# Optimization experiments

Measured on AMD Instinct MI355X. Metric: run time of the kernel, lower is better.

The kernel has to match this reference:

```python
import jax, jax.numpy as jnp
import numpy as np

N = 100000      # nodes
E = 3200000     # edges
G = 1024        # graphs in the batch
D_IN = 128      # input feature dim
H = 64          # hidden dim
BN_EPS = 1e-5


def _linear_init(key, fan_in, shape):
    bound = 1.0 / np.sqrt(fan_in)
    return jax.random.uniform(key, shape, jnp.float32, -bound, bound)


def setup_inputs() -> dict:
    key = jax.random.key(0)
    ks = jax.random.split(key, 16)
    x = jax.random.normal(ks[0], (N, D_IN), jnp.float32)
    edge_index = jax.random.randint(ks[1], (2, E), 0, N, dtype=jnp.int32)
    batch = jnp.sort(jax.random.randint(ks[2], (N,), 0, G, dtype=jnp.int32))
    inp = {"x": x, "edge_index": edge_index, "batch": batch}
    # layer 0 MLP: Linear(D_IN,H) -> ReLU -> BN(H) -> Linear(H,H) -> ReLU
    inp["W1_0"] = _linear_init(ks[3], D_IN, (D_IN, H))
    inp["b1_0"] = _linear_init(ks[4], D_IN, (H,))
    inp["g_0"] = jnp.ones((H,), jnp.float32)
    inp["be_0"] = jnp.zeros((H,), jnp.float32)
    inp["W2_0"] = _linear_init(ks[5], H, (H, H))
    inp["b2_0"] = _linear_init(ks[6], H, (H,))
    # layer 1 MLP: Linear(H,H) -> ReLU -> BN(H) -> Linear(H,H) -> ReLU
    inp["W1_1"] = _linear_init(ks[7], H, (H, H))
    inp["b1_1"] = _linear_init(ks[8], H, (H,))
    inp["g_1"] = jnp.ones((H,), jnp.float32)
    inp["be_1"] = jnp.zeros((H,), jnp.float32)
    inp["W2_1"] = _linear_init(ks[9], H, (H, H))
    inp["b2_1"] = _linear_init(ks[10], H, (H,))
    return inp


def _mlp(h, W1, b1, g, be, W2, b2):
    h = jnp.maximum(h @ W1 + b1, 0.0)
    mu = h.mean(axis=0)                      # BatchNorm1d (training: batch stats)
    var = h.var(axis=0)                      # biased variance, as torch normalizes
    h = g * (h - mu) * jax.lax.rsqrt(var + BN_EPS) + be
    return jnp.maximum(h @ W2 + b2, 0.0)


def _gin(h, src, dst, mlp_params):
    # GINConv, eps=0: out = mlp(x_i + sum_{j->i} x_j)
    agg = jax.ops.segment_sum(h[src], dst, num_segments=N)
    return _mlp(h + agg, *mlp_params)


def reference(x, edge_index, batch,
              W1_0, b1_0, g_0, be_0, W2_0, b2_0,
              W1_1, b1_1, g_1, be_1, W2_1, b2_1):
    src, dst = edge_index[0], edge_index[1]
    h = _gin(x, src, dst, (W1_0, b1_0, g_0, be_0, W2_0, b2_0))
    h = _gin(h, src, dst, (W1_1, b1_1, g_1, be_1, W2_1, b2_1))
    x_g = jax.ops.segment_sum(h, batch, num_segments=G)  # global add pooling
    return (x_g, h)
```

## Files before the change

### kernel.cpp

```cpp
#include <hip/hip_runtime.h>

static inline int cdiv_ll(long long a, long long b){ return (int)((a + b - 1) / b); }

#define EB_CHUNK 8192
#define NPB 256
#define MAXNB 512

__device__ __forceinline__ float bf2f(unsigned short h) {
  unsigned u = (unsigned)h << 16;
  return __uint_as_float(u);
}
__device__ __forceinline__ unsigned short f2bf(float f) {
  unsigned u = __float_as_uint(f);
  u += 0x7FFF + ((u >> 16) & 1);
  return (unsigned short)(u >> 16);
}

template<int K, bool IN_BF16, bool RELU_IN, bool RELU_OUT, bool BIAS, bool OUT_BF16>
__global__ __launch_bounds__(256) void gemm64x64(
    const void* __restrict__ Xv, const float* __restrict__ W,
    const float* __restrict__ bias, void* __restrict__ Yv, int M)
{
  __shared__ float Wl[K * 64];
  __shared__ float XT[64 * 68];
  const float* Xf = (const float*)Xv;
  const unsigned short* Xh = (const unsigned short*)Xv;

  for (int i = threadIdx.x; i < K * 16; i += 256)
    reinterpret_cast<float4*>(Wl)[i] = reinterpret_cast<const float4*>(W)[i];

  const int tr = threadIdx.x >> 4;
  const int tc = threadIdx.x & 15;
  const long long rb = (long long)blockIdx.x * 64;

  float acc[4][4] = {};

  for (int ch = 0; ch < K / 64; ++ch) {
    const int c0 = ch * 64;
    __syncthreads();
    for (int f = threadIdx.x; f < 1024; f += 256) {
      int r = f >> 4, k0 = (f & 15) * 4;
      float4 v = make_float4(0.f, 0.f, 0.f, 0.f);
      if (rb + r < M) {
        if (IN_BF16) {
          ushort4 h = *reinterpret_cast<const ushort4*>(Xh + (rb + r) * K + c0 + k0);
          v.x = bf2f(h.x); v.y = bf2f(h.y); v.z = bf2f(h.z); v.w = bf2f(h.w);
        } else {
          v = *reinterpret_cast<const float4*>(Xf + (rb + r) * K + c0 + k0);
        }
        if (RELU_IN) {
          v.x = fmaxf(v.x, 0.f); v.y = fmaxf(v.y, 0.f);
          v.z = fmaxf(v.z, 0.f); v.w = fmaxf(v.w, 0.f);
        }
      }
      XT[(k0 + 0) * 68 + r] = v.x;
      XT[(k0 + 1) * 68 + r] = v.y;
      XT[(k0 + 2) * 68 + r] = v.z;
      XT[(k0 + 3) * 68 + r] = v.w;
    }
    __syncthreads();
    #pragma unroll 8
    for (int k = 0; k < 64; ++k) {
      float4 xa = *reinterpret_cast<const float4*>(&XT[k * 68 + 4 * tr]);
      float4 wb = *reinterpret_cast<const float4*>(&Wl[(c0 + k) * 64 + 4 * tc]);
      acc[0][0] = fmaf(xa.x, wb.x, acc[0][0]); acc[0][1] = fmaf(xa.x, wb.y, acc[0][1]);
      acc[0][2] = fmaf(xa.x, wb.z, acc[0][2]); acc[0][3] = fmaf(xa.x, wb.w, acc[0][3]);
      acc[1][0] = fmaf(xa.y, wb.x, acc[1][0]); acc[1][1] = fmaf(xa.y, wb.y, acc[1][1]);
      acc[1][2] = fmaf(xa.y, wb.z, acc[1][2]); acc[1][3] = fmaf(xa.y, wb.w, acc[1][3]);
      acc[2][0] = fmaf(xa.z, wb.x, acc[2][0]); acc[2][1] = fmaf(xa.z, wb.y, acc[2][1]);
      acc[2][2] = fmaf(xa.z, wb.z, acc[2][2]); acc[2][3] = fmaf(xa.z, wb.w, acc[2][3]);
      acc[3][0] = fmaf(xa.w, wb.x, acc[3][0]); acc[3][1] = fmaf(xa.w, wb.y, acc[3][1]);
      acc[3][2] = fmaf(xa.w, wb.z, acc[3][2]); acc[3][3] = fmaf(xa.w, wb.w, acc[3][3]);
    }
  }

  float4 bb = make_float4(0.f, 0.f, 0.f, 0.f);
  if (BIAS) bb = *reinterpret_cast<const float4*>(bias + 4 * tc);
  #pragma unroll
  for (int rr = 0; rr < 4; ++rr) {
    long long row = rb + 4 * tr + rr;
    if (row < M) {
      float4 o = make_float4(acc[rr][0] + bb.x, acc[rr][1] + bb.y,
                             acc[rr][2] + bb.z, acc[rr][3] + bb.w);
      if (RELU_OUT) {
        o.x = fmaxf(o.x, 0.f); o.y = fmaxf(o.y, 0.f);
        o.z = fmaxf(o.z, 0.f); o.w = fmaxf(o.w, 0.f);
      }
      if (OUT_BF16) {
        ushort4 h; h.x = f2bf(o.x); h.y = f2bf(o.y); h.z = f2bf(o.z); h.w = f2bf(o.w);
        *reinterpret_cast<ushort4*>((unsigned short*)Yv + row * 64 + 4 * tc) = h;
      } else {
        *reinterpret_cast<float4*>((float*)Yv + row * 64 + 4 * tc) = o;
      }
    }
  }
}

__global__ __launch_bounds__(256) void gemm_dual(
    const float* __restrict__ A, const float* __restrict__ Wa64,
    const float* __restrict__ ba, const float* __restrict__ Wb64,
    unsigned short* __restrict__ P, int M)
{
  __shared__ float Wa[64 * 64];
  __shared__ float Wb[64 * 64];
  __shared__ float XT[64 * 68];
  for (int i = threadIdx.x; i < 1024; i += 256) {
    reinterpret_cast<float4*>(Wa)[i] = reinterpret_cast<const float4*>(Wa64)[i];
    reinterpret_cast<float4*>(Wb)[i] = reinterpret_cast<const float4*>(Wb64)[i];
  }
  const int tr = threadIdx.x >> 4;
  const int tc = threadIdx.x & 15;
  const long long rb = (long long)blockIdx.x * 64;

  for (int f = threadIdx.x; f < 1024; f += 256) {
    int r = f >> 4, k0 = (f & 15) * 4;
    float4 v = make_float4(0.f, 0.f, 0.f, 0.f);
    if (rb + r < M) {
      v = *reinterpret_cast<const float4*>(A + (rb + r) * 64 + k0);
      v.x = fmaxf(v.x, 0.f); v.y = fmaxf(v.y, 0.f);
      v.z = fmaxf(v.z, 0.f); v.w = fmaxf(v.w, 0.f);
    }
    XT[(k0 + 0) * 68 + r] = v.x;
    XT[(k0 + 1) * 68 + r] = v.y;
    XT[(k0 + 2) * 68 + r] = v.z;
    XT[(k0 + 3) * 68 + r] = v.w;
  }
  __syncthreads();

  float acc[4][4] = {};
  #pragma unroll 8
  for (int k = 0; k < 64; ++k) {
    float4 xa = *reinterpret_cast<const float4*>(&XT[k * 68 + 4 * tr]);
    float4 wb = *reinterpret_cast<const float4*>(&Wa[k * 64 + 4 * tc]);
    acc[0][0] = fmaf(xa.x, wb.x, acc[0][0]); acc[0][1] = fmaf(xa.x, wb.y, acc[0][1]);
    acc[0][2] = fmaf(xa.x, wb.z, acc[0][2]); acc[0][3] = fmaf(xa.x, wb.w, acc[0][3]);
    acc[1][0] = fmaf(xa.y, wb.x, acc[1][0]); acc[1][1] = fmaf(xa.y, wb.y, acc[1][1]);
    acc[1][2] = fmaf(xa.y, wb.z, acc[1][2]); acc[1][3] = fmaf(xa.y, wb.w, acc[1][3]);
    acc[2][0] = fmaf(xa.z, wb.x, acc[2][0]); acc[2][1] = fmaf(xa.z, wb.y, acc[2][1]);
    acc[2][2] = fmaf(xa.z, wb.z, acc[2][2]); acc[2][3] = fmaf(xa.z, wb.w, acc[2][3]);
    acc[3][0] = fmaf(xa.w, wb.x, acc[3][0]); acc[3][1] = fmaf(xa.w, wb.y, acc[3][1]);
    acc[3][2] = fmaf(xa.w, wb.z, acc[3][2]); acc[3][3] = fmaf(xa.w, wb.w, acc[3][3]);
  }
  float4 bb = *reinterpret_cast<const float4*>(ba + 4 * tc);
  float h[4][4];
  #pragma unroll
  for (int rr = 0; rr < 4; ++rr) {
    h[rr][0] = fmaxf(acc[rr][0] + bb.x, 0.f);
    h[rr][1] = fmaxf(acc[rr][1] + bb.y, 0.f);
    h[rr][2] = fmaxf(acc[rr][2] + bb.z, 0.f);
    h[rr][3] = fmaxf(acc[rr][3] + bb.w, 0.f);
  }
  __syncthreads();
  #pragma unroll
  for (int cc = 0; cc < 4; ++cc) {
    float4 v = make_float4(h[0][cc], h[1][cc], h[2][cc], h[3][cc]);
    *reinterpret_cast<float4*>(&XT[(4 * tc + cc) * 68 + 4 * tr]) = v;
  }
  __syncthreads();

  float ac2[4][4] = {};
  #pragma unroll 8
  for (int k = 0; k < 64; ++k) {
    float4 xa = *reinterpret_cast<const float4*>(&XT[k * 68 + 4 * tr]);
    float4 wb = *reinterpret_cast<const float4*>(&Wb[k * 64 + 4 * tc]);
    ac2[0][0] = fmaf(xa.x, wb.x, ac2[0][0]); ac2[0][1] = fmaf(xa.x, wb.y, ac2[0][1]);
    ac2[0][2] = fmaf(xa.x, wb.z, ac2[0][2]); ac2[0][3] = fmaf(xa.x, wb.w, ac2[0][3]);
    ac2[1][0] = fmaf(xa.y, wb.x, ac2[1][0]); ac2[1][1] = fmaf(xa.y, wb.y, ac2[1][1]);
    ac2[1][2] = fmaf(xa.y, wb.z, ac2[1][2]); ac2[1][3] = fmaf(xa.y, wb.w, ac2[1][3]);
    ac2[2][0] = fmaf(xa.z, wb.x, ac2[2][0]); ac2[2][1] = fmaf(xa.z, wb.y, ac2[2][1]);
    ac2[2][2] = fmaf(xa.z, wb.z, ac2[2][2]); ac2[2][3] = fmaf(xa.z, wb.w, ac2[2][3]);
    ac2[3][0] = fmaf(xa.w, wb.x, ac2[3][0]); ac2[3][1] = fmaf(xa.w, wb.y, ac2[3][1]);
    ac2[3][2] = fmaf(xa.w, wb.z, ac2[3][2]); ac2[3][3] = fmaf(xa.w, wb.w, ac2[3][3]);
  }
  #pragma unroll
  for (int rr = 0; rr < 4; ++rr) {
    long long row = rb + 4 * tr + rr;
    if (row < M) {
      ushort4 hh;
      hh.x = f2bf(ac2[rr][0]); hh.y = f2bf(ac2[rr][1]);
      hh.z = f2bf(ac2[rr][2]); hh.w = f2bf(ac2[rr][3]);
      *reinterpret_cast<ushort4*>(P + row * 64 + 4 * tc) = hh;
    }
  }
}

__global__ __launch_bounds__(256) void part_hist(
    const int* __restrict__ dst, int* __restrict__ blockHist,
    int E, int NB, int nblocksB)
{
  __shared__ int hist[MAXNB];
  for (int i = threadIdx.x; i < NB; i += 256) hist[i] = 0;
  __syncthreads();
  int base = blockIdx.x * EB_CHUNK;
  int end = min(base + EB_CHUNK, E);
  for (int e = base + threadIdx.x; e < end; e += 256)
    atomicAdd(&hist[dst[e] >> 8], 1);
  __syncthreads();
  for (int i = threadIdx.x; i < NB; i += 256)
    blockHist[(long long)i * nblocksB + blockIdx.x] = hist[i];
}

__global__ __launch_bounds__(256) void scan_bucket_blocks(
    int* __restrict__ blockHist, int* __restrict__ bucketTotal, int nblocksB)
{
  int* row = blockHist + (long long)blockIdx.x * nblocksB;
  __shared__ int tsum[256];
  int v[4]; int local = 0;
  int i0 = threadIdx.x * 4;
  #pragma unroll
  for (int k = 0; k < 4; ++k) { int g = i0 + k; v[k] = (g < nblocksB) ? row[g] : 0; local += v[k]; }
  tsum[threadIdx.x] = local;
  __syncthreads();
  for (int off = 1; off < 256; off <<= 1) {
    int y = (threadIdx.x >= off) ? tsum[threadIdx.x - off] : 0;
    __syncthreads();
    tsum[threadIdx.x] += y;
    __syncthreads();
  }
  int pref = tsum[threadIdx.x] - local;
  #pragma unroll
  for (int k = 0; k < 4; ++k) { int g = i0 + k; if (g < nblocksB) { row[g] = pref; pref += v[k]; } }
  if (threadIdx.x == 255) bucketTotal[blockIdx.x] = tsum[255];
}

__global__ __launch_bounds__(512) void scan_buckets(
    const int* __restrict__ bucketTotal, int* __restrict__ bucketBase, int NB)
{
  __shared__ int tsum[512];
  int t = threadIdx.x;
  int v = (t < NB) ? bucketTotal[t] : 0;
  tsum[t] = v;
  __syncthreads();
  for (int off = 1; off < 512; off <<= 1) {
    int y = (t >= off) ? tsum[t - off] : 0;
    __syncthreads();
    tsum[t] += y;
    __syncthreads();
  }
  if (t < NB) bucketBase[t] = tsum[t] - v;
  if (t == NB - 1) bucketBase[NB] = tsum[t];
}

__global__ __launch_bounds__(256) void part_scatter(
    const int* __restrict__ src, const int* __restrict__ dst,
    const int* __restrict__ blockHist, const int* __restrict__ bucketBase,
    unsigned* __restrict__ ebuf, int E, int NB, int nblocksB)
{
  __shared__ int cursor[MAXNB];
  for (int i = threadIdx.x; i < NB; i += 256)
    cursor[i] = bucketBase[i] + blockHist[(long long)i * nblocksB + blockIdx.x];
  __syncthreads();
  int base = blockIdx.x * EB_CHUNK;
  int end = min(base + EB_CHUNK, E);
  for (int e = base + threadIdx.x; e < end; e += 256) {
    int s = src[e], d = dst[e];
    int p = atomicAdd(&cursor[d >> 8], 1);
    ebuf[p] = (unsigned)s | ((unsigned)(d & (NPB - 1)) << 24);
  }
}

__global__ __launch_bounds__(256) void bucket_csr(
    const unsigned* __restrict__ ebuf, const int* __restrict__ bucketBase,
    int* __restrict__ rowptr, int* __restrict__ col, int N, int NB)
{
  int b = blockIdx.x;
  int eb = bucketBase[b], ee = bucketBase[b + 1];
  int nodeBase = b * NPB;
  __shared__ int hist[NPB];
  __shared__ int tsum[NPB];
  __shared__ int cur[NPB];
  hist[threadIdx.x] = 0;
  __syncthreads();
  for (int e = eb + threadIdx.x; e < ee; e += 256)
    atomicAdd(&hist[ebuf[e] >> 24], 1);
  __syncthreads();
  int local = hist[threadIdx.x];
  tsum[threadIdx.x] = local;
  __syncthreads();
  for (int off = 1; off < 256; off <<= 1) {
    int y = (threadIdx.x >= off) ? tsum[threadIdx.x - off] : 0;
    __syncthreads();
    tsum[threadIdx.x] += y;
    __syncthreads();
  }
  int pref = tsum[threadIdx.x] - local;
  int node = nodeBase + threadIdx.x;
  if (node < N) rowptr[node] = eb + pref;
  if (b == NB - 1 && threadIdx.x == 0) rowptr[N] = ee;
  cur[threadIdx.x] = pref;
  __syncthreads();
  for (int e = eb + threadIdx.x; e < ee; e += 256) {
    unsigned w = ebuf[e];
    int l = (int)(w >> 24);
    int p = eb + atomicAdd(&cur[l], 1);
    col[p] = (int)(w & 0xFFFFFFu);
  }
}

__global__ __launch_bounds__(256) void gin_gather_bf16(
    const int* __restrict__ rowptr, const int* __restrict__ col,
    const unsigned short* __restrict__ P, const float* __restrict__ b1,
    float* __restrict__ A, float* __restrict__ stats, int N, int nodeStride)
{
  const int lane = threadIdx.x & 63;
  const int wv = threadIdx.x >> 6;
  const int q = lane >> 4;
  const int cl = lane & 15;
  float s[4] = {0.f, 0.f, 0.f, 0.f};
  float sq[4] = {0.f, 0.f, 0.f, 0.f};
  const float4 bb = *reinterpret_cast<const float4*>(b1 + 4 * cl);

  for (int node = blockIdx.x * 4 + wv; node < N; node += nodeStride) {
    const int beg = rowptr[node], end = rowptr[node + 1];
    float a0 = 0.f, a1 = 0.f, a2 = 0.f, a3 = 0.f;
    if (q == 1) {
      ushort4 h = *reinterpret_cast<const ushort4*>(P + (long long)node * 64 + 4 * cl);
      a0 = bf2f(h.x); a1 = bf2f(h.y); a2 = bf2f(h.z); a3 = bf2f(h.w);
    } else if (q == 2) {
      a0 = bb.x; a1 = bb.y; a2 = bb.z; a3 = bb.w;
    }
    int j = beg + q;
    for (; j + 12 < end; j += 16) {
      int rA = col[j], rB = col[j + 4], rC = col[j + 8], rD = col[j + 12];
      ushort4 hA = *reinterpret_cast<const ushort4*>(P + (long long)rA * 64 + 4 * cl);
      ushort4 hB = *reinterpret_cast<const ushort4*>(P + (long long)rB * 64 + 4 * cl);
      ushort4 hC = *reinterpret_cast<const ushort4*>(P + (long long)rC * 64 + 4 * cl);
      ushort4 hD = *reinterpret_cast<const ushort4*>(P + (long long)rD * 64 + 4 * cl);
      a0 += bf2f(hA.x); a1 += bf2f(hA.y); a2 += bf2f(hA.z); a3 += bf2f(hA.w);
      a0 += bf2f(hB.x); a1 += bf2f(hB.y); a2 += bf2f(hB.z); a3 += bf2f(hB.w);
      a0 += bf2f(hC.x); a1 += bf2f(hC.y); a2 += bf2f(hC.z); a3 += bf2f(hC.w);
      a0 += bf2f(hD.x); a1 += bf2f(hD.y); a2 += bf2f(hD.z); a3 += bf2f(hD.w);
    }
    for (; j < end; j += 4) {
      int rA = col[j];
      ushort4 hA = *reinterpret_cast<const ushort4*>(P + (long long)rA * 64 + 4 * cl);
      a0 += bf2f(hA.x); a1 += bf2f(hA.y); a2 += bf2f(hA.z); a3 += bf2f(hA.w);
    }
    a0 += __shfl_xor(a0, 16); a0 += __shfl_xor(a0, 32);
    a1 += __shfl_xor(a1, 16); a1 += __shfl_xor(a1, 32);
    a2 += __shfl_xor(a2, 16); a2 += __shfl_xor(a2, 32);
    a3 += __shfl_xor(a3, 16); a3 += __shfl_xor(a3, 32);
    if (q == 0) {
      *reinterpret_cast<float4*>(A + (long long)node * 64 + 4 * cl) =
          make_float4(a0, a1, a2, a3);
    } else if (q == 1) {
      float r0 = fmaxf(a0, 0.f), r1 = fmaxf(a1, 0.f);
      float r2 = fmaxf(a2, 0.f), r3 = fmaxf(a3, 0.f);
      s[0] += r0; s[1] += r1; s[2] += r2; s[3] += r3;
      sq[0] += r0 * r0; sq[1] += r1 * r1; sq[2] += r2 * r2; sq[3] += r3 * r3;
    }
  }

  __shared__ float st[4][16][8];
  if (q == 1) {
    st[wv][cl][0] = s[0]; st[wv][cl][1] = s[1]; st[wv][cl][2] = s[2]; st[wv][cl][3] = s[3];
    st[wv][cl][4] = sq[0]; st[wv][cl][5] = sq[1]; st[wv][cl][6] = sq[2]; st[wv][cl][7] = sq[3];
  }
  __syncthreads();
  if (threadIdx.x < 128) {
    int c = threadIdx.x;
    int colid = c & 63, part = c >> 6;
    int idx = (part ? 4 : 0) + (colid & 3);
    float v = st[0][colid >> 2][idx] + st[1][colid >> 2][idx]
            + st[2][colid >> 2][idx] + st[3][colid >> 2][idx];
    atomicAdd(&stats[c], v);
  }
}

__global__ void bn_fold(
    const float* __restrict__ stats, const float* __restrict__ g, const float* __restrict__ be,
    const float* __restrict__ W2, const float* __restrict__ b2,
    float* __restrict__ W2f, float* __restrict__ b2f, float invN)
{
  int j = threadIdx.x;
  __shared__ float sc[64], sh[64];
  float mu = stats[j] * invN;
  float var = stats[64 + j] * invN - mu * mu;
  float s = g[j] * rsqrtf(var + 1e-5f);
  sc[j] = s;
  sh[j] = be[j] - mu * s;
  __syncthreads();
  float acc = b2[j];
  for (int k = 0; k < 64; ++k) {
    float w = W2[k * 64 + j];
    W2f[k * 64 + j] = sc[k] * w;
    acc += sh[k] * w;
  }
  b2f[j] = acc;
}

__global__ __launch_bounds__(256) void pool_sorted(
    const float* __restrict__ Hf, const int* __restrict__ batch,
    float* __restrict__ out, int N, int G)
{
  int g = blockIdx.x * 4 + (threadIdx.x >> 6);
  int c = threadIdx.x & 63;
  if (g >= G) return;
  int lo = 0, hi = N;
  while (lo < hi) { int mid = (lo + hi) >> 1; if (batch[mid] < g) lo = mid + 1; else hi = mid; }
  int beg = lo;
  hi = N;
  while (lo < hi) { int mid = (lo + hi) >> 1; if (batch[mid] < g + 1) lo = mid + 1; else hi = mid; }
  int end = lo;
  float acc = 0.f;
  for (int r = beg; r < end; ++r) acc += Hf[(long long)r * 64 + c];
  out[(long long)g * 64 + c] = acc;
}

extern "C" void kernel_launch(void* const* d_in, const int* in_sizes, int n_in,
                              void* d_out, int out_size, void* d_ws, size_t ws_size,
                              hipStream_t stream) {
  const float* x      = (const float*)d_in[0];
  const int*   ei     = (const int*)d_in[1];
  const int*   batch  = (const int*)d_in[2];
  const float* W1_0 = (const float*)d_in[3];
  const float* b1_0 = (const float*)d_in[4];
  const float* g_0  = (const float*)d_in[5];
  const float* be_0 = (const float*)d_in[6];
  const float* W2_0 = (const float*)d_in[7];
  const float* b2_0 = (const float*)d_in[8];
  const float* W1_1 = (const float*)d_in[9];
  const float* b1_1 = (const float*)d_in[10];
  const float* g_1  = (const float*)d_in[11];
  const float* be_1 = (const float*)d_in[12];
  const float* W2_1 = (const float*)d_in[13];
  const float* b2_1 = (const float*)d_in[14];

  const int N = in_sizes[0] / 128;
  const int E = in_sizes[1] / 2;
  const int G = (out_size - N * 64) / 64;
  const int* srcI = ei;
  const int* dstI = ei + E;

  float* outG = (float*)d_out;
  float* outH = (float*)d_out + (long long)G * 64;

  const int NB = cdiv_ll(N, NPB);
  const int nblocksB = cdiv_ll(E, EB_CHUNK);

  char* w = (char*)d_ws;
  size_t r2 = (size_t)E * 4;
  if ((size_t)N * 64 * 2 > r2) r2 = (size_t)N * 64 * 2;
  unsigned* ebuf        = (unsigned*)w;
  unsigned short* Pbuf  = (unsigned short*)w;
  w += r2;
  int* col       = (int*)w; w += (size_t)E * 4;
  int* rowptr    = (int*)w; w += (size_t)(N + 1) * 4;
  int* blockHist = (int*)w; w += (size_t)NB * nblocksB * 4;
  int* bucketTotal = (int*)w; w += (size_t)NB * 4;
  int* bucketBase  = (int*)w; w += (size_t)(NB + 1) * 4;
  float* stats0 = (float*)w; w += 128 * 4;
  float* stats1 = (float*)w; w += 128 * 4;
  float* W2f0   = (float*)w; w += 64 * 64 * 4;
  float* b2f0   = (float*)w; w += 64 * 4;
  float* W2f1   = (float*)w; w += 64 * 64 * 4;
  float* b2f1   = (float*)w; w += 64 * 4;

  const int gemmGrid = cdiv_ll(N, 64);
  const int gatherGrid = 2048;

  hipMemsetAsync(stats0, 0, 256 * sizeof(float), stream);

  part_hist<<<nblocksB, 256, 0, stream>>>(dstI, blockHist, E, NB, nblocksB);
  scan_bucket_blocks<<<NB, 256, 0, stream>>>(blockHist, bucketTotal, nblocksB);
  scan_buckets<<<1, 512, 0, stream>>>(bucketTotal, bucketBase, NB);
  part_scatter<<<nblocksB, 256, 0, stream>>>(srcI, dstI, blockHist, bucketBase, ebuf, E, NB, nblocksB);
  bucket_csr<<<NB, 256, 0, stream>>>(ebuf, bucketBase, rowptr, col, N, NB);

  gemm64x64<128, false, false, false, false, true><<<gemmGrid, 256, 0, stream>>>(x, W1_0, nullptr, Pbuf, N);
  gin_gather_bf16<<<gatherGrid, 256, 0, stream>>>(rowptr, col, Pbuf, b1_0, outH, stats0, N, gatherGrid * 4);
  bn_fold<<<1, 64, 0, stream>>>(stats0, g_0, be_0, W2_0, b2_0, W2f0, b2f0, 1.0f / N);
  gemm_dual<<<gemmGrid, 256, 0, stream>>>(outH, W2f0, b2f0, W1_1, Pbuf, N);

  gin_gather_bf16<<<gatherGrid, 256, 0, stream>>>(rowptr, col, Pbuf, b1_1, outH, stats1, N, gatherGrid * 4);
  bn_fold<<<1, 64, 0, stream>>>(stats1, g_1, be_1, W2_1, b2_1, W2f1, b2f1, 1.0f / N);
  gemm64x64<64, false, true, true, true, false><<<gemmGrid, 256, 0, stream>>>(outH, W2f1, b2f1, outH, N);

  pool_sorted<<<cdiv_ll(G, 4), 256, 0, stream>>>(outH, batch, outG, N, G);
}
```

Before: 440.0 us.

## Switch dense GEMMs to bf16 MFMA and cache CSR bucket edges in LDS

Replaces the scalar fp32 FMA GEMM kernels with bf16 MFMA 16x16x32 kernels. Inputs and weights are converted to bf16 in swizzled LDS tiles, so the GEMMs run on the matrix cores. Separately, bucket_csr stages each bucket's edges in LDS when they fit, which avoids reading ebuf from global memory twice. The cost is reduced precision: inputs and the intermediate hidden layer in the dual GEMM are rounded to bf16, where before they were fp32.

```diff
diff --git a/kernel.cpp b/kernel.cpp
--- a/kernel.cpp
+++ b/kernel.cpp
@@ -5,6 +5,10 @@
 #define EB_CHUNK 8192
 #define NPB 256
 #define MAXNB 512
+#define CSR_LDS 10240
+
+typedef short bf16x8 __attribute__((ext_vector_type(8)));
+typedef float f32x4 __attribute__((ext_vector_type(4)));
 
 __device__ __forceinline__ float bf2f(unsigned short h) {
   unsigned u = (unsigned)h << 16;
@@ -16,170 +20,134 @@
   return (unsigned short)(u >> 16);
 }
 
-template<int K, bool IN_BF16, bool RELU_IN, bool RELU_OUT, bool BIAS, bool OUT_BF16>
-__global__ __launch_bounds__(256) void gemm64x64(
-    const void* __restrict__ Xv, const float* __restrict__ W,
-    const float* __restrict__ bias, void* __restrict__ Yv, int M)
-{
-  __shared__ float Wl[K * 64];
-  __shared__ float XT[64 * 68];
-  const float* Xf = (const float*)Xv;
-  const unsigned short* Xh = (const unsigned short*)Xv;
-
-  for (int i = threadIdx.x; i < K * 16; i += 256)
-    reinterpret_cast<float4*>(Wl)[i] = reinterpret_cast<const float4*>(W)[i];
-
-  const int tr = threadIdx.x >> 4;
-  const int tc = threadIdx.x & 15;
-  const long long rb = (long long)blockIdx.x * 64;
-
-  float acc[4][4] = {};
-
-  for (int ch = 0; ch < K / 64; ++ch) {
-    const int c0 = ch * 64;
-    __syncthreads();
-    for (int f = threadIdx.x; f < 1024; f += 256) {
-      int r = f >> 4, k0 = (f & 15) * 4;
-      float4 v = make_float4(0.f, 0.f, 0.f, 0.f);
-      if (rb + r < M) {
-        if (IN_BF16) {
-          ushort4 h = *reinterpret_cast<const ushort4*>(Xh + (rb + r) * K + c0 + k0);
-          v.x = bf2f(h.x); v.y = bf2f(h.y); v.z = bf2f(h.z); v.w = bf2f(h.w);
-        } else {
-          v = *reinterpret_cast<const float4*>(Xf + (rb + r) * K + c0 + k0);
-        }
-        if (RELU_IN) {
-          v.x = fmaxf(v.x, 0.f); v.y = fmaxf(v.y, 0.f);
-          v.z = fmaxf(v.z, 0.f); v.w = fmaxf(v.w, 0.f);
-        }
-      }
-      XT[(k0 + 0) * 68 + r] = v.x;
-      XT[(k0 + 1) * 68 + r] = v.y;
-      XT[(k0 + 2) * 68 + r] = v.z;
-      XT[(k0 + 3) * 68 + r] = v.w;
-    }
-    __syncthreads();
-    #pragma unroll 8
-    for (int k = 0; k < 64; ++k) {
-      float4 xa = *reinterpret_cast<const float4*>(&XT[k * 68 + 4 * tr]);
-      float4 wb = *reinterpret_cast<const float4*>(&Wl[(c0 + k) * 64 + 4 * tc]);
-      acc[0][0] = fmaf(xa.x, wb.x, acc[0][0]); acc[0][1] = fmaf(xa.x, wb.y, acc[0][1]);
-      acc[0][2] = fmaf(xa.x, wb.z, acc[0][2]); acc[0][3] = fmaf(xa.x, wb.w, acc[0][3]);
-      acc[1][0] = fmaf(xa.y, wb.x, acc[1][0]); acc[1][1] = fmaf(xa.y, wb.y, acc[1][1]);
-      acc[1][2] = fmaf(xa.y, wb.z, acc[1][2]); acc[1][3] = fmaf(xa.y, wb.w, acc[1][3]);
-      acc[2][0] = fmaf(xa.z, wb.x, acc[2][0]); acc[2][1] = fmaf(xa.z, wb.y, acc[2][1]);
-      acc[2][2] = fmaf(xa.z, wb.z, acc[2][2]); acc[2][3] = fmaf(xa.z, wb.w, acc[2][3]);
-      acc[3][0] = fmaf(xa.w, wb.x, acc[3][0]); acc[3][1] = fmaf(xa.w, wb.y, acc[3][1]);
-      acc[3][2] = fmaf(xa.w, wb.z, acc[3][2]); acc[3][3] = fmaf(xa.w, wb.w, acc[3][3]);
-    }
-  }
-
-  float4 bb = make_float4(0.f, 0.f, 0.f, 0.f);
-  if (BIAS) bb = *reinterpret_cast<const float4*>(bias + 4 * tc);
-  #pragma unroll
-  for (int rr = 0; rr < 4; ++rr) {
-    long long row = rb + 4 * tr + rr;
-    if (row < M) {
-      float4 o = make_float4(acc[rr][0] + bb.x, acc[rr][1] + bb.y,
-                             acc[rr][2] + bb.z, acc[rr][3] + bb.w);
-      if (RELU_OUT) {
-        o.x = fmaxf(o.x, 0.f); o.y = fmaxf(o.y, 0.f);
-        o.z = fmaxf(o.z, 0.f); o.w = fmaxf(o.w, 0.f);
-      }
-      if (OUT_BF16) {
-        ushort4 h; h.x = f2bf(o.x); h.y = f2bf(o.y); h.z = f2bf(o.z); h.w = f2bf(o.w);
-        *reinterpret_cast<ushort4*>((unsigned short*)Yv + row * 64 + 4 * tc) = h;
-      } else {
-        *reinterpret_cast<float4*>((float*)Yv + row * 64 + 4 * tc) = o;
-      }
-    }
-  }
-}
-
-__global__ __launch_bounds__(256) void gemm_dual(
-    const float* __restrict__ A, const float* __restrict__ Wa64,
-    const float* __restrict__ ba, const float* __restrict__ Wb64,
-    unsigned short* __restrict__ P, int M)
-{
-  __shared__ float Wa[64 * 64];
-  __shared__ float Wb[64 * 64];
-  __shared__ float XT[64 * 68];
-  for (int i = threadIdx.x; i < 1024; i += 256) {
-    reinterpret_cast<float4*>(Wa)[i] = reinterpret_cast<const float4*>(Wa64)[i];
-    reinterpret_cast<float4*>(Wb)[i] = reinterpret_cast<const float4*>(Wb64)[i];
-  }
-  const int tr = threadIdx.x >> 4;
-  const int tc = threadIdx.x & 15;
-  const long long rb = (long long)blockIdx.x * 64;
-
-  for (int f = threadIdx.x; f < 1024; f += 256) {
-    int r = f >> 4, k0 = (f & 15) * 4;
+#define SWZ(row, byteoff) ((byteoff) ^ (((row) & 7) << 4))
+
+template<int K, bool RELU>
+__device__ __forceinline__ void stage_x_bf16(
+    char* XlB, const float* __restrict__ X, long long rb, int M)
+{
+  for (int f = threadIdx.x; f < 16 * K; f += 256) {
+    int r = f / (K / 4), c4 = (f % (K / 4)) * 4;
     float4 v = make_float4(0.f, 0.f, 0.f, 0.f);
     if (rb + r < M) {
-      v = *reinterpret_cast<const float4*>(A + (rb + r) * 64 + k0);
-      v.x = fmaxf(v.x, 0.f); v.y = fmaxf(v.y, 0.f);
-      v.z = fmaxf(v.z, 0.f); v.w = fmaxf(v.w, 0.f);
-    }
-    XT[(k0 + 0) * 68 + r] = v.x;
-    XT[(k0 + 1) * 68 + r] = v.y;
-    XT[(k0 + 2) * 68 + r] = v.z;
-    XT[(k0 + 3) * 68 + r] = v.w;
-  }
-  __syncthreads();
-
-  float acc[4][4] = {};
-  #pragma unroll 8
-  for (int k = 0; k < 64; ++k) {
-    float4 xa = *reinterpret_cast<const float4*>(&XT[k * 68 + 4 * tr]);
-    float4 wb = *reinterpret_cast<const float4*>(&Wa[k * 64 + 4 * tc]);
-    acc[0][0] = fmaf(xa.x, wb.x, acc[0][0]); acc[0][1] = fmaf(xa.x, wb.y, acc[0][1]);
-    acc[0][2] = fmaf(xa.x, wb.z, acc[0][2]); acc[0][3] = fmaf(xa.x, wb.w, acc[0][3]);
-    acc[1][0] = fmaf(xa.y, wb.x, acc[1][0]); acc[1][1] = fmaf(xa.y, wb.y, acc[1][1]);
-    acc[1][2] = fmaf(xa.y, wb.z, acc[1][2]); acc[1][3] = fmaf(xa.y, wb.w, acc[1][3]);
-    acc[2][0] = fmaf(xa.z, wb.x, acc[2][0]); acc[2][1] = fmaf(xa.z, wb.y, acc[2][1]);
-    acc[2][2] = fmaf(xa.z, wb.z, acc[2][2]); acc[2][3] = fmaf(xa.z, wb.w, acc[2][3]);
-    acc[3][0] = fmaf(xa.w, wb.x, acc[3][0]); acc[3][1] = fmaf(xa.w, wb.y, acc[3][1]);
-    acc[3][2] = fmaf(xa.w, wb.z, acc[3][2]); acc[3][3] = fmaf(xa.w, wb.w, acc[3][3]);
-  }
-  float4 bb = *reinterpret_cast<const float4*>(ba + 4 * tc);
-  float h[4][4];
-  #pragma unroll
-  for (int rr = 0; rr < 4; ++rr) {
-    h[rr][0] = fmaxf(acc[rr][0] + bb.x, 0.f);
-    h[rr][1] = fmaxf(acc[rr][1] + bb.y, 0.f);
-    h[rr][2] = fmaxf(acc[rr][2] + bb.z, 0.f);
-    h[rr][3] = fmaxf(acc[rr][3] + bb.w, 0.f);
-  }
-  __syncthreads();
-  #pragma unroll
-  for (int cc = 0; cc < 4; ++cc) {
-    float4 v = make_float4(h[0][cc], h[1][cc], h[2][cc], h[3][cc]);
-    *reinterpret_cast<float4*>(&XT[(4 * tc + cc) * 68 + 4 * tr]) = v;
-  }
-  __syncthreads();
-
-  float ac2[4][4] = {};
-  #pragma unroll 8
-  for (int k = 0; k < 64; ++k) {
-    float4 xa = *reinterpret_cast<const float4*>(&XT[k * 68 + 4 * tr]);
-    float4 wb = *reinterpret_cast<const float4*>(&Wb[k * 64 + 4 * tc]);
-    ac2[0][0] = fmaf(xa.x, wb.x, ac2[0][0]); ac2[0][1] = fmaf(xa.x, wb.y, ac2[0][1]);
-    ac2[0][2] = fmaf(xa.x, wb.z, ac2[0][2]); ac2[0][3] = fmaf(xa.x, wb.w, ac2[0][3]);
-    ac2[1][0] = fmaf(xa.y, wb.x, ac2[1][0]); ac2[1][1] = fmaf(xa.y, wb.y, ac2[1][1]);
-    ac2[1][2] = fmaf(xa.y, wb.z, ac2[1][2]); ac2[1][3] = fmaf(xa.y, wb.w, ac2[1][3]);
-    ac2[2][0] = fmaf(xa.z, wb.x, ac2[2][0]); ac2[2][1] = fmaf(xa.z, wb.y, ac2[2][1]);
-    ac2[2][2] = fmaf(xa.z, wb.z, ac2[2][2]); ac2[2][3] = fmaf(xa.z, wb.w, ac2[2][3]);
-    ac2[3][0] = fmaf(xa.w, wb.x, ac2[3][0]); ac2[3][1] = fmaf(xa.w, wb.y, ac2[3][1]);
-    ac2[3][2] = fmaf(xa.w, wb.z, ac2[3][2]); ac2[3][3] = fmaf(xa.w, wb.w, ac2[3][3]);
-  }
-  #pragma unroll
-  for (int rr = 0; rr < 4; ++rr) {
-    long long row = rb + 4 * tr + rr;
-    if (row < M) {
-      ushort4 hh;
-      hh.x = f2bf(ac2[rr][0]); hh.y = f2bf(ac2[rr][1]);
-      hh.z = f2bf(ac2[rr][2]); hh.w = f2bf(ac2[rr][3]);
-      *reinterpret_cast<ushort4*>(P + row * 64 + 4 * tc) = hh;
+      v = *reinterpret_cast<const float4*>(X + (rb + r) * K + c4);
+      if (RELU) {
+        v.x = fmaxf(v.x, 0.f); v.y = fmaxf(v.y, 0.f);
+        v.z = fmaxf(v.z, 0.f); v.w = fmaxf(v.w, 0.f);
+      }
+    }
+    ushort4 h; h.x = f2bf(v.x); h.y = f2bf(v.y); h.z = f2bf(v.z); h.w = f2bf(v.w);
+    *reinterpret_cast<ushort4*>(XlB + r * (2 * K) + SWZ(r, c4 * 2)) = h;
+  }
+}
+
+template<int K>
+__device__ __forceinline__ void stage_wt_bf16(char* WTB, const float* __restrict__ W)
+{
+  for (int t = threadIdx.x; t < K * 32; t += 256) {
+    int c = t & 63, kp = t >> 6;
+    float w0 = W[(2 * kp) * 64 + c];
+    float w1 = W[(2 * kp + 1) * 64 + c];
+    ushort2 hh; hh.x = f2bf(w0); hh.y = f2bf(w1);
+    *reinterpret_cast<ushort2*>(WTB + c * (2 * K) + SWZ(c, 4 * kp)) = hh;
+  }
+}
+
+template<int K>
+__device__ __forceinline__ void mfma_chain(
+    f32x4* acc, const char* XlB, const char* WTB, int wv, int lr, int lg)
+{
+  const int rowb = 16 * wv + lr;
+  #pragma unroll
+  for (int kc = 0; kc < K / 32; ++kc) {
+    const int kByte = kc * 64 + lg * 16;
+    bf16x8 a = *reinterpret_cast<const bf16x8*>(XlB + rowb * (2 * K) + SWZ(rowb, kByte));
+    #pragma unroll
+    for (int ct = 0; ct < 4; ++ct) {
+      int c = ct * 16 + lr;
+      bf16x8 b = *reinterpret_cast<const bf16x8*>(WTB + c * (2 * K) + SWZ(c, kByte));
+      acc[ct] = __builtin_amdgcn_mfma_f32_16x16x32_bf16(a, b, acc[ct], 0, 0, 0);
+    }
+  }
+}
+
+template<int K, bool IN_RELU, bool RELU_OUT, bool BIAS, bool OUT_BF16>
+__global__ __launch_bounds__(256) void mfma_gemm(
+    const float* __restrict__ X, const float* __restrict__ W,
+    const float* __restrict__ bias, void* __restrict__ Yv, int M)
+{
+  __shared__ __align__(16) char XlB[64 * 2 * K];
+  __shared__ __align__(16) char WTB[64 * 2 * K];
+  const long long rb = (long long)blockIdx.x * 64;
+  stage_x_bf16<K, IN_RELU>(XlB, X, rb, M);
+  stage_wt_bf16<K>(WTB, W);
+  __syncthreads();
+
+  const int lane = threadIdx.x & 63, wv = threadIdx.x >> 6;
+  const int lr = lane & 15, lg = lane >> 4;
+  f32x4 acc[4] = {};
+  mfma_chain<K>(acc, XlB, WTB, wv, lr, lg);
+
+  #pragma unroll
+  for (int ct = 0; ct < 4; ++ct) {
+    const int c = ct * 16 + lr;
+    const float bv = BIAS ? bias[c] : 0.0f;
+    #pragma unroll
+    for (int j = 0; j < 4; ++j) {
+      long long row = rb + 16 * wv + lg * 4 + j;
+      if (row < M) {
+        float v = acc[ct][j] + bv;
+        if (RELU_OUT) v = fmaxf(v, 0.f);
+        if (OUT_BF16) ((unsigned short*)Yv)[row * 64 + c] = f2bf(v);
+        else          ((float*)Yv)[row * 64 + c] = v;
+      }
+    }
+  }
+}
+
+__global__ __launch_bounds__(256) void mfma_dual(
+    const float* __restrict__ A, const float* __restrict__ Wa,
+    const float* __restrict__ ba, const float* __restrict__ Wb,
+    unsigned short* __restrict__ P, int M)
+{
+  __shared__ __align__(16) char XlB[64 * 128];
+  __shared__ __align__(16) char WTaB[64 * 128];
+  __shared__ __align__(16) char WTbB[64 * 128];
+  __shared__ __align__(16) char Xl2B[64 * 128];
+  const long long rb = (long long)blockIdx.x * 64;
+  stage_x_bf16<64, true>(XlB, A, rb, M);
+  stage_wt_bf16<64>(WTaB, Wa);
+  stage_wt_bf16<64>(WTbB, Wb);
+  __syncthreads();
+
+  const int lane = threadIdx.x & 63, wv = threadIdx.x >> 6;
+  const int lr = lane & 15, lg = lane >> 4;
+  f32x4 acc[4] = {};
+  mfma_chain<64>(acc, XlB, WTaB, wv, lr, lg);
+
+  #pragma unroll
+  for (int ct = 0; ct < 4; ++ct) {
+    const int c = ct * 16 + lr;
+    const float bv = ba[c];
+    #pragma unroll
+    for (int j = 0; j < 4; ++j) {
+      int rloc = 16 * wv + lg * 4 + j;
+      float v = fmaxf(acc[ct][j] + bv, 0.f);
+      *reinterpret_cast<unsigned short*>(Xl2B + rloc * 128 + SWZ(rloc, c * 2)) = f2bf(v);
+    }
+  }
+  __syncthreads();
+
+  f32x4 ac2[4] = {};
+  mfma_chain<64>(ac2, Xl2B, WTbB, wv, lr, lg);
+
+  #pragma unroll
+  for (int ct = 0; ct < 4; ++ct) {
+    const int c = ct * 16 + lr;
+    #pragma unroll
+    for (int j = 0; j < 4; ++j) {
+      long long row = rb + 16 * wv + lg * 4 + j;
+      if (row < M) P[row * 64 + c] = f2bf(ac2[ct][j]);
     }
   }
 }
@@ -265,14 +233,18 @@
 {
   int b = blockIdx.x;
   int eb = bucketBase[b], ee = bucketBase[b + 1];
+  int cnt = ee - eb;
   int nodeBase = b * NPB;
+  __shared__ unsigned ebl[CSR_LDS];
   __shared__ int hist[NPB];
   __shared__ int tsum[NPB];
   __shared__ int cur[NPB];
+  const bool fit = (cnt <= CSR_LDS);
   hist[threadIdx.x] = 0;
-  __syncthreads();
-  for (int e = eb + threadIdx.x; e < ee; e += 256)
-    atomicAdd(&hist[ebuf[e] >> 24], 1);
+  if (fit) for (int i = threadIdx.x; i < cnt; i += 256) ebl[i] = ebuf[eb + i];
+  __syncthreads();
+  for (int i = threadIdx.x; i < cnt; i += 256)
+    atomicAdd(&hist[(fit ? ebl[i] : ebuf[eb + i]) >> 24], 1);
   __syncthreads();
   int local = hist[threadIdx.x];
   tsum[threadIdx.x] = local;
@@ -289,8 +261,8 @@
   if (b == NB - 1 && threadIdx.x == 0) rowptr[N] = ee;
   cur[threadIdx.x] = pref;
   __syncthreads();
-  for (int e = eb + threadIdx.x; e < ee; e += 256) {
-    unsigned w = ebuf[e];
+  for (int i = threadIdx.x; i < cnt; i += 256) {
+    unsigned w = fit ? ebl[i] : ebuf[eb + i];
     int l = (int)(w >> 24);
     int p = eb + atomicAdd(&cur[l], 1);
     col[p] = (int)(w & 0xFFFFFFu);
@@ -467,14 +439,14 @@
   part_scatter<<<nblocksB, 256, 0, stream>>>(srcI, dstI, blockHist, bucketBase, ebuf, E, NB, nblocksB);
   bucket_csr<<<NB, 256, 0, stream>>>(ebuf, bucketBase, rowptr, col, N, NB);
 
-  gemm64x64<128, false, false, false, false, true><<<gemmGrid, 256, 0, stream>>>(x, W1_0, nullptr, Pbuf, N);
+  mfma_gemm<128, false, false, false, true><<<gemmGrid, 256, 0, stream>>>(x, W1_0, nullptr, Pbuf, N);
   gin_gather_bf16<<<gatherGrid, 256, 0, stream>>>(rowptr, col, Pbuf, b1_0, outH, stats0, N, gatherGrid * 4);
   bn_fold<<<1, 64, 0, stream>>>(stats0, g_0, be_0, W2_0, b2_0, W2f0, b2f0, 1.0f / N);
-  gemm_dual<<<gemmGrid, 256, 0, stream>>>(outH, W2f0, b2f0, W1_1, Pbuf, N);
+  mfma_dual<<<gemmGrid, 256, 0, stream>>>(outH, W2f0, b2f0, W1_1, Pbuf, N);
 
   gin_gather_bf16<<<gatherGrid, 256, 0, stream>>>(rowptr, col, Pbuf, b1_1, outH, stats1, N, gatherGrid * 4);
   bn_fold<<<1, 64, 0, stream>>>(stats1, g_1, be_1, W2_1, b2_1, W2f1, b2f1, 1.0f / N);
-  gemm64x64<64, false, true, true, true, false><<<gemmGrid, 256, 0, stream>>>(outH, W2f1, b2f1, outH, N);
+  mfma_gemm<64, true, true, true, false><<<gemmGrid, 256, 0, stream>>>(outH, W2f1, b2f1, outH, N);
 
   pool_sorted<<<cdiv_ll(G, 4), 256, 0, stream>>>(outH, batch, outG, N, G);
 }
```

After: 408.2 us. 1.08x faster.
